# Performance work log

Hardware: AMD Instinct MI355X
Metric: run time of the kernel (lower is better)

The kernel has to match this reference:

```python
import jax, jax.numpy as jnp
import numpy as np

N_NODES = 100000
N_EDGES = 1600000
D_FEAT = 64
H1 = 16
H2 = 1


def setup_inputs() -> dict:
    key = jax.random.key(0)
    ks = jax.random.split(key, 8)
    x = jax.random.normal(ks[0], (N_NODES, D_FEAT), dtype=jnp.float32)
    edge_index = jax.random.randint(ks[1], (2, N_EDGES), 0, N_NODES, dtype=jnp.int64)
    s1 = 1.0 / np.sqrt(D_FEAT)
    s2 = 1.0 / np.sqrt(H1)
    Wl1 = jax.random.uniform(ks[2], (H1, D_FEAT), jnp.float32, -s1, s1)
    Wr1 = jax.random.uniform(ks[3], (H1, D_FEAT), jnp.float32, -s1, s1)
    b1 = jax.random.uniform(ks[4], (H1,), jnp.float32, -s1, s1)
    Wl2 = jax.random.uniform(ks[5], (H2, H1), jnp.float32, -s2, s2)
    Wr2 = jax.random.uniform(ks[6], (H2, H1), jnp.float32, -s2, s2)
    b2 = jax.random.uniform(ks[7], (H2,), jnp.float32, -s2, s2)
    return {"x": x, "edge_index": edge_index, "Wl1": Wl1, "Wr1": Wr1, "b1": b1,
            "Wl2": Wl2, "Wr2": Wr2, "b2": b2}


def _sage_conv(h, src, dst, Wl, Wr, b, n_nodes):
    # mean aggregation of source-node features onto destination nodes
    msg_sum = jax.ops.segment_sum(h[src], dst, num_segments=n_nodes)  # [N, d]
    cnt = jax.ops.segment_sum(jnp.ones((src.shape[0],), h.dtype), dst,
                              num_segments=n_nodes)  # [N]
    mean = msg_sum / jnp.maximum(cnt, 1.0)[:, None]
    # out = lin_l(mean_neighbors) + lin_r(self) + bias
    return mean @ Wl.T + h @ Wr.T + b


def reference(x, edge_index, Wl1, Wr1, b1, Wl2, Wr2, b2):
    src, dst = edge_index[0], edge_index[1]
    n = x.shape[0]
    h = jax.nn.relu(_sage_conv(x, src, dst, Wl1, Wr1, b1, n))
    # F.dropout(training=False) is identity at inference
    out = _sage_conv(h, src, dst, Wl2, Wr2, b2, n)
    return out
```

## Files before the change

### kernel.cpp

```cpp
#include <hip/hip_runtime.h>
#include <hip/hip_fp16.h>

#define H1F 16
#define BSH 8
#define BNODES 256
#define MAXBUCK 512
#define CAPSH 13
#define CAPB (1 << CAPSH)
#define SSH 10
#define TILE 8192
#define MAXPT 16

struct Params {
    const float* x;
    const float* Wl1; const float* Wr1; const float* b1;
    const float* Wl2; const float* Wr2; const float* b2;
    const int* ei;
    int* cur8;
    unsigned int* edge2;
    int* csr; int* offp; int* degv;
    __half* xl; float* xr; float* hl2; float* outp;
    float* out;
    int N, E, nPart, nProj, nbuck;
};

union SharedU {
    struct {
        int lhist[MAXBUCK];
        int lbase[MAXBUCK];
        int gbase[MAXBUCK];
        int wsum[8];
        unsigned int stage[TILE];
    } p;
    struct {
        float4 wl4[16][17];
        float4 wr4[16][17];
    } q;
};

__device__ __forceinline__ void do_part(const Params& P, int vb, SharedU& sh) {
    int t = threadIdx.x;
    int shard = vb & 7;
    sh.p.lhist[t] = 0;
    __syncthreads();

    int E = P.E;
    int e0 = vb * TILE;

#pragma unroll
    for (int batch = 0; batch < 2; ++batch) {
        int eb = e0 + batch * 4096 + t * 8;
        if (eb + 8 <= E) {
            int4 d0 = *(const int4*)(P.ei + E + eb);
            int4 d1 = *(const int4*)(P.ei + E + eb + 4);
            atomicAdd(&sh.p.lhist[d0.x >> BSH], 1);
            atomicAdd(&sh.p.lhist[d0.y >> BSH], 1);
            atomicAdd(&sh.p.lhist[d0.z >> BSH], 1);
            atomicAdd(&sh.p.lhist[d0.w >> BSH], 1);
            atomicAdd(&sh.p.lhist[d1.x >> BSH], 1);
            atomicAdd(&sh.p.lhist[d1.y >> BSH], 1);
            atomicAdd(&sh.p.lhist[d1.z >> BSH], 1);
            atomicAdd(&sh.p.lhist[d1.w >> BSH], 1);
        } else {
#pragma unroll
            for (int k = 0; k < 8; ++k) {
                int e = eb + k;
                if (e < E) atomicAdd(&sh.p.lhist[P.ei[E + e] >> BSH], 1);
            }
        }
    }
    __syncthreads();

    int v = sh.p.lhist[t];
    if (v > 0)
        sh.p.gbase[t] = (t << CAPSH) + (shard << SSH) +
                        atomicAdd(&P.cur8[shard * MAXBUCK + t], (v + 3) & ~3);
    int lane = t & 63, wid = t >> 6;
    int s = v;
#pragma unroll
    for (int d = 1; d < 64; d <<= 1) {
        int u = __shfl_up(s, d);
        if (lane >= d) s += u;
    }
    if (lane == 63) sh.p.wsum[wid] = s;
    __syncthreads();
    int wofs = 0;
    for (int w = 0; w < wid; ++w) wofs += sh.p.wsum[w];
    int myBase = wofs + s - v;
    sh.p.lbase[t] = myBase;
    sh.p.lhist[t] = myBase;
    __syncthreads();

#pragma unroll
    for (int batch = 0; batch < 2; ++batch) {
        int eb = e0 + batch * 4096 + t * 8;
        if (eb + 8 <= E) {
            int4 s0 = *(const int4*)(P.ei + eb);
            int4 s1 = *(const int4*)(P.ei + eb + 4);
            int4 d0 = *(const int4*)(P.ei + E + eb);
            int4 d1 = *(const int4*)(P.ei + E + eb + 4);
            int ssv[8] = {s0.x, s0.y, s0.z, s0.w, s1.x, s1.y, s1.z, s1.w};
            int ddv[8] = {d0.x, d0.y, d0.z, d0.w, d1.x, d1.y, d1.z, d1.w};
#pragma unroll
            for (int k = 0; k < 8; ++k) {
                int b = ddv[k] >> BSH;
                int pos = atomicAdd(&sh.p.lhist[b], 1);
                sh.p.stage[pos] = ((unsigned int)ssv[k] << BSH) |
                                  (unsigned int)(ddv[k] & (BNODES - 1));
            }
        } else {
#pragma unroll
            for (int k = 0; k < 8; ++k) {
                int e = eb + k;
                if (e < E) {
                    int src = P.ei[e];
                    int dst = P.ei[E + e];
                    int b = dst >> BSH;
                    int pos = atomicAdd(&sh.p.lhist[b], 1);
                    sh.p.stage[pos] = ((unsigned int)src << BSH) |
                                      (unsigned int)(dst & (BNODES - 1));
                }
            }
        }
    }
    __syncthreads();

    int lb = sh.p.lbase[t];
    int cntB = sh.p.lhist[t] - lb;
    if (cntB > 0) {
        int gb = sh.p.gbase[t];
        int subEnd = (t << CAPSH) + ((shard + 1) << SSH);
        int padded = (cntB + 3) & ~3;
        int jmax = subEnd - gb;
        if (padded > jmax) padded = jmax;
        for (int j = 0; j < padded; j += 4) {
            int4 v4;
            v4.x = (j + 0 < cntB) ? (int)sh.p.stage[lb + j + 0] : -1;
            v4.y = (j + 1 < cntB) ? (int)sh.p.stage[lb + j + 1] : -1;
            v4.z = (j + 2 < cntB) ? (int)sh.p.stage[lb + j + 2] : -1;
            v4.w = (j + 3 < cntB) ? (int)sh.p.stage[lb + j + 3] : -1;
            *(int4*)(P.edge2 + gb + j) = v4;
        }
    }
}

__device__ __forceinline__ void do_proj(const Params& P, int pvb, SharedU& sh) {
    int t = threadIdx.x;
    if (t < 256) {
        sh.q.wl4[t >> 4][t & 15] = ((const float4*)P.Wl1)[t];
    } else {
        int u = t - 256;
        sh.q.wr4[u >> 4][u & 15] = ((const float4*)P.Wr1)[u];
    }
    __syncthreads();

    int f = t & 15;
    int nl = t >> 4;
    float bf = P.b1[f];
    const float4* x4 = (const float4*)P.x;

#pragma unroll
    for (int rep = 0; rep < 4; ++rep) {
        int gn = pvb * 128 + rep * 32 + nl;
        if (gn < P.N) {
            float al = 0.0f, ar = 0.0f;
#pragma unroll
            for (int k4 = 0; k4 < 16; ++k4) {
                float4 xv = x4[(size_t)gn * 16 + k4];
                float4 a = sh.q.wl4[f][k4];
                float4 b = sh.q.wr4[f][k4];
                al += xv.x * a.x + xv.y * a.y + xv.z * a.z + xv.w * a.w;
                ar += xv.x * b.x + xv.y * b.y + xv.z * b.z + xv.w * b.w;
            }
            P.xl[(size_t)gn * H1F + f] = __float2half(al);
            P.xr[(size_t)gn * H1F + f] = ar + bf;
        }
    }
}

__global__ __launch_bounds__(512) void kA(Params P) {
    __shared__ SharedU sh;
    int vb = blockIdx.x;
    if (vb < P.nPart) do_part(P, vb, sh);
    else do_proj(P, vb - P.nPart, sh);
}

__global__ __launch_bounds__(512) void kBC(Params P) {
    __shared__ int sorted[CAPB];
    __shared__ int hh[BNODES];
    __shared__ int ofs[BNODES];
    __shared__ int dgs[BNODES];
    __shared__ int wsum[4];

    int t = threadIdx.x;
    int b = blockIdx.x;
    int n0 = b << BSH;
    int e0 = b << CAPSH;

    if (t < BNODES) hh[t] = 0;
    __syncthreads();

    int cnt = 0;
    unsigned int rw[MAXPT];
#pragma unroll
    for (int s = 0; s < 8; ++s) {
        int c = P.cur8[s * MAXBUCK + b];
        if (c > (1 << SSH)) c = (1 << SSH);
        cnt += c;
        int base = e0 + (s << SSH);
#pragma unroll
        for (int k = 0; k < 2; ++k) {
            int idx = (k << 9) + t;
            rw[s * 2 + k] = (idx < c) ? P.edge2[base + idx] : 0xFFFFFFFFu;
        }
    }

#pragma unroll
    for (int k = 0; k < MAXPT; ++k)
        if (rw[k] != 0xFFFFFFFFu) atomicAdd(&hh[rw[k] & (BNODES - 1)], 1);
    __syncthreads();

    int lane = t & 63, wid = t >> 6;
    int v = 0, s = 0;
    if (t < BNODES) {
        v = hh[t];
        s = v;
#pragma unroll
        for (int d = 1; d < 64; d <<= 1) {
            int u = __shfl_up(s, d);
            if (lane >= d) s += u;
        }
        if (lane == 63) wsum[wid] = s;
    }
    __syncthreads();
    if (t < BNODES) {
        int wofs = 0;
        for (int w = 0; w < wid; ++w) wofs += wsum[w];
        int excl = wofs + s - v;
        ofs[t] = excl;
        dgs[t] = v;
        int gn = n0 + t;
        if (gn < P.N) {
            P.degv[gn] = v;
            P.offp[gn] = e0 + excl;
        }
        hh[t] = excl;
    }
    __syncthreads();

#pragma unroll
    for (int k = 0; k < MAXPT; ++k) {
        if (rw[k] != 0xFFFFFFFFu) {
            int d = (int)(rw[k] & (BNODES - 1));
            int pos = atomicAdd(&hh[d], 1);
            sorted[pos] = (int)(rw[k] >> BSH);
        }
    }
    __syncthreads();

    for (int i = t; i < cnt; i += 512) P.csr[e0 + i] = sorted[i];

    const __half2* xl2 = (const __half2*)P.xl;
    const float2* xr2 = (const float2*)P.xr;
    int l = t & 7;
    int nb = t >> 3;
    float2 wlv = ((const float2*)P.Wl2)[l];
    float2 wrv = ((const float2*)P.Wr2)[l];
    float bias2 = P.b2[0];

#pragma unroll
    for (int sub = 0; sub < 4; ++sub) {
        int nl = sub * 64 + nb;
        int node = n0 + nl;
        if (node < P.N) {
            int start = ofs[nl];
            int d = dgs[nl];
            float sx = 0.0f, sy = 0.0f;
            int j = 0;
            for (; j + 4 <= d; j += 4) {
                int s0 = sorted[start + j], s1 = sorted[start + j + 1];
                int s2 = sorted[start + j + 2], s3 = sorted[start + j + 3];
                float2 v0 = __half22float2(xl2[(size_t)s0 * 8 + l]);
                float2 v1 = __half22float2(xl2[(size_t)s1 * 8 + l]);
                float2 v2 = __half22float2(xl2[(size_t)s2 * 8 + l]);
                float2 v3 = __half22float2(xl2[(size_t)s3 * 8 + l]);
                sx += v0.x + v1.x + v2.x + v3.x;
                sy += v0.y + v1.y + v2.y + v3.y;
            }
            for (; j < d; ++j) {
                float2 vv = __half22float2(xl2[(size_t)sorted[start + j] * 8 + l]);
                sx += vv.x; sy += vv.y;
            }

            float inv = 1.0f / fmaxf((float)d, 1.0f);
            float2 xrv = xr2[(size_t)node * 8 + l];
            float h0 = fmaxf(sx * inv + xrv.x, 0.0f);
            float h1 = fmaxf(sy * inv + xrv.y, 0.0f);
            float pl = h0 * wlv.x + h1 * wlv.y;
            float pr = h0 * wrv.x + h1 * wrv.y;
#pragma unroll
            for (int off = 4; off; off >>= 1) {
                pl += __shfl_xor(pl, off);
                pr += __shfl_xor(pr, off);
            }
            if (l == 0) {
                P.hl2[node] = pl;
                P.outp[node] = pr + bias2;
            }
        }
    }
}

__global__ __launch_bounds__(512) void kD(Params P) {
    int g = blockIdx.x;
    int xcd = g & 7, r = g >> 3;
    int bi = r >> 1, k = r & 1;
    int b = bi * 8 + xcd;
    if (b >= P.nbuck) return;
    int t = threadIdx.x;
    int node = (b << BSH) + (k << 7) + (t >> 2);
    int l = t & 3;
    if (node >= P.N) return;

    int d = P.degv[node];
    const int* row = P.csr + P.offp[node];

    float s = 0.0f;
    for (int j = l; j < d; j += 4) s += P.hl2[row[j]];
    s += __shfl_xor(s, 1);
    s += __shfl_xor(s, 2);
    if (l == 0) P.out[node] = s / fmaxf((float)d, 1.0f) + P.outp[node];
}

extern "C" void kernel_launch(void* const* d_in, const int* in_sizes, int n_in,
                              void* d_out, int out_size, void* d_ws, size_t ws_size,
                              hipStream_t stream) {
    Params P;
    P.x   = (const float*)d_in[0];
    P.ei  = (const int*)d_in[1];
    P.Wl1 = (const float*)d_in[2];
    P.Wr1 = (const float*)d_in[3];
    P.b1  = (const float*)d_in[4];
    P.Wl2 = (const float*)d_in[5];
    P.Wr2 = (const float*)d_in[6];
    P.b2  = (const float*)d_in[7];
    P.out = (float*)d_out;

    P.N = in_sizes[0] / 64;
    P.E = in_sizes[1] / 2;
    P.nbuck = (P.N + BNODES - 1) >> BSH;
    P.nPart = (P.E + TILE - 1) / TILE;
    P.nProj = (P.N + 127) / 128;

    size_t win = (size_t)P.nbuck << CAPSH;
    P.cur8  = (int*)d_ws;
    P.edge2 = (unsigned int*)(P.cur8 + 8 * MAXBUCK);
    P.csr   = (int*)(P.edge2 + win);
    P.offp  = P.csr + win;
    P.degv  = P.offp + P.N;
    P.xl    = (__half*)(P.degv + P.N);
    P.xr    = (float*)(P.xl + (size_t)16 * P.N);
    P.hl2   = P.xr + (size_t)16 * P.N;
    P.outp  = P.hl2 + P.N;

    (void)hipMemsetAsync(P.cur8, 0, 8 * MAXBUCK * sizeof(int), stream);

    kA<<<P.nPart + P.nProj, 512, 0, stream>>>(P);
    kBC<<<P.nbuck, 512, 0, stream>>>(P);
    int gridD = 8 * ((P.nbuck + 7) / 8) * 2;
    kD<<<gridD, 512, 0, stream>>>(P);
}
```

Measured before the change: 64.97 us.

## Drop CSR materialization; aggregate layer-2 with shared-memory atomics from bucketed edges

```diff
diff --git a/kernel.cpp b/kernel.cpp
--- a/kernel.cpp
+++ b/kernel.cpp
@@ -18,7 +18,7 @@
     const int* ei;
     int* cur8;
     unsigned int* edge2;
-    int* csr; int* offp; int* degv;
+    int* degv;
     __half* xl; float* xr; float* hl2; float* outp;
     float* out;
     int N, E, nPart, nProj, nbuck;
@@ -200,13 +200,11 @@
     if (t < BNODES) hh[t] = 0;
     __syncthreads();
 
-    int cnt = 0;
     unsigned int rw[MAXPT];
 #pragma unroll
     for (int s = 0; s < 8; ++s) {
         int c = P.cur8[s * MAXBUCK + b];
         if (c > (1 << SSH)) c = (1 << SSH);
-        cnt += c;
         int base = e0 + (s << SSH);
 #pragma unroll
         for (int k = 0; k < 2; ++k) {
@@ -240,10 +238,7 @@
         ofs[t] = excl;
         dgs[t] = v;
         int gn = n0 + t;
-        if (gn < P.N) {
-            P.degv[gn] = v;
-            P.offp[gn] = e0 + excl;
-        }
+        if (gn < P.N) P.degv[gn] = v;
         hh[t] = excl;
     }
     __syncthreads();
@@ -257,8 +252,6 @@
         }
     }
     __syncthreads();
-
-    for (int i = t; i < cnt; i += 512) P.csr[e0 + i] = sorted[i];
 
     const __half2* xl2 = (const __half2*)P.xl;
     const float2* xr2 = (const float2*)P.xr;
@@ -312,24 +305,37 @@
 }
 
 __global__ __launch_bounds__(512) void kD(Params P) {
-    int g = blockIdx.x;
-    int xcd = g & 7, r = g >> 3;
-    int bi = r >> 1, k = r & 1;
-    int b = bi * 8 + xcd;
-    if (b >= P.nbuck) return;
+    __shared__ float acc2[BNODES];
     int t = threadIdx.x;
-    int node = (b << BSH) + (k << 7) + (t >> 2);
-    int l = t & 3;
-    if (node >= P.N) return;
-
-    int d = P.degv[node];
-    const int* row = P.csr + P.offp[node];
-
-    float s = 0.0f;
-    for (int j = l; j < d; j += 4) s += P.hl2[row[j]];
-    s += __shfl_xor(s, 1);
-    s += __shfl_xor(s, 2);
-    if (l == 0) P.out[node] = s / fmaxf((float)d, 1.0f) + P.outp[node];
+    int b = blockIdx.x;
+    int n0 = b << BSH;
+    int e0 = b << CAPSH;
+
+    if (t < BNODES) acc2[t] = 0.0f;
+    __syncthreads();
+
+#pragma unroll
+    for (int s = 0; s < 8; ++s) {
+        int c = P.cur8[s * MAXBUCK + b];
+        if (c > (1 << SSH)) c = (1 << SSH);
+        int base = e0 + (s << SSH);
+#pragma unroll
+        for (int k = 0; k < 2; ++k) {
+            int idx = (k << 9) + t;
+            if (idx < c) {
+                unsigned int u = P.edge2[base + idx];
+                if (u != 0xFFFFFFFFu)
+                    atomicAdd(&acc2[u & (BNODES - 1)], P.hl2[u >> BSH]);
+            }
+        }
+    }
+    __syncthreads();
+
+    if (t < BNODES) {
+        int gn = n0 + t;
+        if (gn < P.N)
+            P.out[gn] = acc2[t] / fmaxf((float)P.degv[gn], 1.0f) + P.outp[gn];
+    }
 }
 
 extern "C" void kernel_launch(void* const* d_in, const int* in_sizes, int n_in,
@@ -355,9 +361,7 @@
     size_t win = (size_t)P.nbuck << CAPSH;
     P.cur8  = (int*)d_ws;
     P.edge2 = (unsigned int*)(P.cur8 + 8 * MAXBUCK);
-    P.csr   = (int*)(P.edge2 + win);
-    P.offp  = P.csr + win;
-    P.degv  = P.offp + P.N;
+    P.degv  = (int*)(P.edge2 + win);
     P.xl    = (__half*)(P.degv + P.N);
     P.xr    = (float*)(P.xl + (size_t)16 * P.N);
     P.hl2   = P.xr + (size_t)16 * P.N;
@@ -367,6 +371,5 @@
 
     kA<<<P.nPart + P.nProj, 512, 0, stream>>>(P);
     kBC<<<P.nbuck, 512, 0, stream>>>(P);
-    int gridD = 8 * ((P.nbuck + 7) / 8) * 2;
-    kD<<<gridD, 512, 0, stream>>>(P);
-}
+    kD<<<P.nbuck, 512, 0, stream>>>(P);
+}
```

Result: slower. 67.04 us (+3.2%).
